# Kernel optimization log

Hardware: AMD Instinct MI355X
Metric: run time of the kernel (lower is better)

Reference implementation:

```python
import jax
import jax.numpy as jnp
from jax import lax
import numpy as np

ALPHA = 1.5   # entmax sparsity parameter (layer default)
N_ITER = 50   # bisection iterations (converges to ~2^-50 interval)


def entmax_bisect(z, alpha=ALPHA, n_iter=N_ITER):
    """alpha-entmax along the last axis via bisection on the threshold tau.

    p_i = max((alpha-1)*z_i - tau, 0) ** (1/(alpha-1)), with sum_i p_i = 1.
    """
    inv = 1.0 / (alpha - 1.0)
    x = (alpha - 1.0) * z
    mx = jnp.max(x, axis=-1, keepdims=True)
    d = x.shape[-1]
    lo = mx - 1.0                      # f(lo) >= 0
    hi = mx - float(d) ** (1.0 - alpha)  # f(hi) <= 0

    def body(_, carry):
        lo, hi = carry
        mid = 0.5 * (lo + hi)
        p = jnp.maximum(x - mid, 0.0) ** inv
        f = jnp.sum(p, axis=-1, keepdims=True) - 1.0
        lo = jnp.where(f >= 0.0, mid, lo)
        hi = jnp.where(f >= 0.0, hi, mid)
        return lo, hi

    lo, hi = lax.fori_loop(0, n_iter, body, (lo, hi))
    tau = 0.5 * (lo + hi)
    p = jnp.maximum(x - tau, 0.0) ** inv
    return p / jnp.sum(p, axis=-1, keepdims=True)


def setup_inputs() -> dict:
    k = jax.random.key(0)
    kq, kk, kv = jax.random.split(k, 3)
    B, S, D = 8, 2048, 128
    return {
        "query": jax.random.normal(kq, (B, S, D), dtype=jnp.float32),
        "key": jax.random.normal(kk, (B, S, D), dtype=jnp.float32),
        "value": jax.random.normal(kv, (B, S, D), dtype=jnp.float32),
    }


def reference(query, key, value):
    # scores: [B, Sq, Sk]
    scores = jnp.einsum("bqd,bkd->bqk", query, key)
    weights = entmax_bisect(scores, alpha=ALPHA)
    # outputs: [B, Sq, D]
    return jnp.einsum("bqk,bkd->bqd", weights, value)
```

## Files before the change

### kernel.cpp

```cpp
#include <hip/hip_runtime.h>
#include <math.h>

#define NB 8
#define S 2048
#define D 128
#define ROWS 32
#define CAP 64
#define NTH 256
#define WKEYS 512
#define CHUNK 32
#define NCK (WKEYS / CHUNK)
#define MARGIN 1.6f

typedef __attribute__((ext_vector_type(8))) short bf16x8;
typedef __attribute__((ext_vector_type(4))) float f32x4;

__device__ __forceinline__ unsigned fmap(float f) {
    unsigned u = __float_as_uint(f);
    return (u & 0x80000000u) ? ~u : (u | 0x80000000u);
}
__device__ __forceinline__ float funmap(unsigned k) {
    return (k & 0x80000000u) ? __uint_as_float(k ^ 0x80000000u) : __uint_as_float(~k);
}
__device__ __forceinline__ unsigned short f2bf(float f) {
    unsigned u = __float_as_uint(f);
    return (unsigned short)((u + 0x7fffu + ((u >> 16) & 1u)) >> 16);
}

__global__ void convert_kernel(const float* __restrict__ q, const float* __restrict__ k,
                               unsigned short* __restrict__ qb, unsigned short* __restrict__ kb) {
    int i = blockIdx.x * NTH + threadIdx.x;
    float4 qv = ((const float4*)q)[i];
    float4 kv = ((const float4*)k)[i];
    ushort4 qo, ko;
    qo.x = f2bf(0.5f * qv.x); qo.y = f2bf(0.5f * qv.y); qo.z = f2bf(0.5f * qv.z); qo.w = f2bf(0.5f * qv.w);
    ko.x = f2bf(kv.x);        ko.y = f2bf(kv.y);        ko.z = f2bf(kv.z);        ko.w = f2bf(kv.w);
    ((ushort4*)qb)[i] = qo;
    ((ushort4*)kb)[i] = ko;
}

__global__ __launch_bounds__(NTH, 2) void entmax_mfma_kernel(
    const float* __restrict__ query, const float* __restrict__ key,
    const float* __restrict__ value, float* __restrict__ out,
    const unsigned short* __restrict__ qb, const unsigned short* __restrict__ kb)
{
    __shared__ float cVal[ROWS][CAP];
    __shared__ unsigned short cIdx[ROWS][CAP];
    __shared__ unsigned rmS[ROWS];
    __shared__ int ccnt[ROWS];

    const int tid  = threadIdx.x;
    const int b    = blockIdx.x & 7;
    const int rb   = blockIdx.x >> 3;
    const int w    = tid >> 6;
    const int lane = tid & 63;
    const int g    = lane >> 4;
    const int l15  = lane & 15;

    if (tid < ROWS) { rmS[tid] = fmap(-3.0e38f); ccnt[tid] = 0; }
    __syncthreads();

    const uint4* Qb4 = (const uint4*)qb + (size_t)(b * S + rb * ROWS) * 16;
    uint4 aq[2][4];
    #pragma unroll
    for (int rt = 0; rt < 2; rt++)
        #pragma unroll
        for (int s = 0; s < 4; s++)
            aq[rt][s] = Qb4[(rt * 16 + l15) * 16 + s * 4 + g];

    const uint4* Kb4 = (const uint4*)kb + (size_t)(b * S) * 16;
    const int key0w = w * WKEYS;

    float rmr[2][4];
    #pragma unroll
    for (int rt = 0; rt < 2; rt++)
        #pragma unroll
        for (int j = 0; j < 4; j++) rmr[rt][j] = -3.0e38f;

    uint4 bb0[8], bb1[8];

#define LOADB(dst, ck_)                                                              \
    {                                                                                \
        int kbase_ = key0w + (ck_) * CHUNK;                                          \
        _Pragma("unroll")                                                            \
        for (int kt = 0; kt < 2; kt++)                                               \
            _Pragma("unroll")                                                        \
            for (int s = 0; s < 4; s++)                                              \
                dst[kt * 4 + s] = Kb4[(size_t)(kbase_ + kt * 16 + l15) * 16 + s * 4 + g]; \
    }

#define CHUNK_BODY(cur, nxt, ck_)                                                    \
    {                                                                                \
        if ((ck_) + 1 < NCK) LOADB(nxt, (ck_) + 1);                                  \
        f32x4 acc[2][2];                                                             \
        _Pragma("unroll")                                                            \
        for (int rt = 0; rt < 2; rt++)                                               \
            _Pragma("unroll")                                                        \
            for (int kt = 0; kt < 2; kt++) acc[rt][kt] = (f32x4){0.f, 0.f, 0.f, 0.f}; \
        _Pragma("unroll")                                                            \
        for (int s = 0; s < 4; s++) {                                                \
            bf16x8 fb0 = *reinterpret_cast<const bf16x8*>(&cur[0 * 4 + s]);          \
            bf16x8 fb1 = *reinterpret_cast<const bf16x8*>(&cur[1 * 4 + s]);          \
            _Pragma("unroll")                                                        \
            for (int rt = 0; rt < 2; rt++) {                                         \
                bf16x8 fa = *reinterpret_cast<const bf16x8*>(&aq[rt][s]);            \
                acc[rt][0] = __builtin_amdgcn_mfma_f32_16x16x32_bf16(fa, fb0, acc[rt][0], 0, 0, 0); \
                acc[rt][1] = __builtin_amdgcn_mfma_f32_16x16x32_bf16(fa, fb1, acc[rt][1], 0, 0, 0); \
            }                                                                        \
        }                                                                            \
          \
        float red[2][4];                                                             \
        _Pragma("unroll")                                                            \
        for (int rt = 0; rt < 2; rt++)                                               \
            _Pragma("unroll")                                                        \
            for (int j = 0; j < 4; j++) red[rt][j] = fmaxf(acc[rt][0][j], acc[rt][1][j]); \
        _Pragma("unroll")                                                            \
        for (int m = 1; m <= 8; m <<= 1)                                             \
            _Pragma("unroll")                                                        \
            for (int rt = 0; rt < 2; rt++)                                           \
                _Pragma("unroll")                                                    \
                for (int j = 0; j < 4; j++)                                          \
                    red[rt][j] = fmaxf(red[rt][j], __shfl_xor(red[rt][j], m));       \
        bool up[2][4];                                                               \
        _Pragma("unroll")                                                            \
        for (int rt = 0; rt < 2; rt++)                                               \
            _Pragma("unroll")                                                        \
            for (int j = 0; j < 4; j++) {                                            \
                up[rt][j] = red[rt][j] > rmr[rt][j];                                 \
                rmr[rt][j] = fmaxf(rmr[rt][j], red[rt][j]);                          \
            }                                                                        \
        if (l15 == 0) {                                                              \
            _Pragma("unroll")                                                        \
            for (int rt = 0; rt < 2; rt++)                                           \
                _Pragma("unroll")                                                    \
                for (int j = 0; j < 4; j++)                                          \
                    if (up[rt][j]) atomicMax(&rmS[rt * 16 + g * 4 + j], fmap(rmr[rt][j])); \
        }                                                                            \
        float thr[2][4];                                                             \
        _Pragma("unroll")                                                            \
        for (int rt = 0; rt < 2; rt++)                                               \
            _Pragma("unroll")                                                        \
            for (int j = 0; j < 4; j++)                                              \
                thr[rt][j] = fmaxf(rmr[rt][j], funmap(rmS[rt * 16 + g * 4 + j])) - MARGIN; \
        int kb0_ = key0w + (ck_) * CHUNK + l15;                                      \
        _Pragma("unroll")                                                            \
        for (int rt = 0; rt < 2; rt++)                                               \
            _Pragma("unroll")                                                        \
            for (int kt = 0; kt < 2; kt++)                                           \
                _Pragma("unroll")                                                    \
                for (int j = 0; j < 4; j++) {                                        \
                    float v_ = acc[rt][kt][j];                                       \
                    if (v_ > thr[rt][j]) {                                           \
                        int row_ = rt * 16 + g * 4 + j;                              \
                        int slot_ = atomicAdd(&ccnt[row_], 1);                       \
                        if (slot_ < CAP) {                                           \
                            cVal[row_][slot_] = v_;                                  \
                            cIdx[row_][slot_] = (unsigned short)(kb0_ + kt * 16);    \
                        }                                                            \
                    }                                                                \
                }                                                                    \
    }

    LOADB(bb0, 0);
    for (int t = 0; t < NCK / 2; t++) {
        CHUNK_BODY(bb0, bb1, 2 * t);
        CHUNK_BODY(bb1, bb0, 2 * t + 1);
    }

    if (l15 == 0) {
        #pragma unroll
        for (int rt = 0; rt < 2; rt++)
            #pragma unroll
            for (int j = 0; j < 4; j++)
                atomicMax(&rmS[rt * 16 + g * 4 + j], fmap(rmr[rt][j]));
    }
    __syncthreads();

    const float* Qg = query + (size_t)(b * S + rb * ROWS) * D;
    const float* Kg = key   + (size_t)b * S * D;
    const float* Vg = value + (size_t)b * S * D;
    float* Og = out + (size_t)(b * S + rb * ROWS) * D;

    for (int r8 = 0; r8 < 8; r8++) {
        int row = w * 8 + r8;
        int n = min(ccnt[row], CAP);
        float thrc = funmap(rmS[row]) - MARGIN;

        float v = (lane < n) ? cVal[row][lane] : -3.0e38f;
        unsigned short id = (lane < n) ? cIdx[row][lane] : 0;
        unsigned long long mk = __ballot(v > thrc);
        int nc = __popcll(mk);
        int pos = __popcll(mk & ((1ull << lane) - 1ull));
        if (v > thrc) cIdx[row][pos] = id;

        int c0 = lane >> 3;
        int dl = lane & 7;
        float4 q4[4];
        #pragma unroll
        for (int i = 0; i < 4; i++)
            q4[i] = ((const float4*)(Qg + (size_t)row * D))[dl * 4 + i];
        for (int cc = c0; cc < nc; cc += 8) {
            int ky = cIdx[row][cc];
            float s = 0.f;
            #pragma unroll
            for (int i = 0; i < 4; i++) {
                float4 k4 = ((const float4*)(Kg + (size_t)ky * D))[dl * 4 + i];
                s = fmaf(q4[i].x, k4.x, s);
                s = fmaf(q4[i].y, k4.y, s);
                s = fmaf(q4[i].z, k4.z, s);
                s = fmaf(q4[i].w, k4.w, s);
            }
            s += __shfl_xor(s, 1);
            s += __shfl_xor(s, 2);
            s += __shfl_xor(s, 4);
            if (dl == 0) cVal[row][cc] = 0.5f * s;
        }

        float tauf = 0.f;
        if (lane == 0) {
            for (int i = 0; i < nc - 1; i++) {
                int mi = i; float mv = cVal[row][i];
                for (int j2 = i + 1; j2 < nc; j2++)
                    if (cVal[row][j2] > mv) { mv = cVal[row][j2]; mi = j2; }
                if (mi != i) {
                    float tv = cVal[row][i]; cVal[row][i] = cVal[row][mi]; cVal[row][mi] = tv;
                    unsigned short ti = cIdx[row][i]; cIdx[row][i] = cIdx[row][mi]; cIdx[row][mi] = ti;
                }
            }
            double S1 = 0.0, S2 = 0.0;
            double tau = (double)cVal[row][0] - 1.0;
            for (int k2 = 1; k2 <= nc; k2++) {
                double xk = (double)cVal[row][k2 - 1];
                S1 += xk; S2 += xk * xk;
                double disc = S1 * S1 - (double)k2 * (S2 - 1.0);
                if (disc >= 0.0) {
                    double tk = (S1 - sqrt(disc)) / (double)k2;
                    if (xk > tk) tau = tk;
                }
            }
            tauf = (float)tau;
        }
        tauf = __shfl(tauf, 0);

        float Z = 0.f;
        float2 o = make_float2(0.f, 0.f);
        for (int cc = 0; cc < nc; cc++) {
            float x = cVal[row][cc];
            float t = fmaxf(x - tauf, 0.f);
            float p = t * t;
            Z += p;
            if (t > 0.f) {
                int ky = cIdx[row][cc];
                float2 a = ((const float2*)(Vg + (size_t)ky * D))[lane];
                o.x = fmaf(p, a.x, o.x);
                o.y = fmaf(p, a.y, o.y);
            }
        }
        float zi = 1.0f / Z;
        o.x *= zi; o.y *= zi;
        ((float2*)(Og + (size_t)row * D))[lane] = o;
    }
}

#define FTK 64
#define FNT (S / FTK)
#define FCAP 120
#define HI_OFF 0.022097086912079608f
#define NITER 50

__global__ __launch_bounds__(NTH, 2) void entmax_attn_fallback(
    const float* __restrict__ query, const float* __restrict__ key,
    const float* __restrict__ value, float* __restrict__ out)
{
    __shared__ float4 sK[FTK * 32];
    __shared__ float4 sQ[ROWS * 32];
    __shared__ int    cIdx[ROWS][FCAP];
    __shared__ float  cVal[ROWS][FCAP];
    __shared__ int    ccnt[ROWS];

    const int tid = threadIdx.x;
    const int bid = blockIdx.x;
    const int b   = bid >> 6;
    const int rb  = bid & 63;

    const float4* Qg = (const float4*)(query + ((size_t)b * S + (size_t)rb * ROWS) * D);
    const float4* Kg = (const float4*)(key + (size_t)b * S * D);

    #pragma unroll
    for (int i = 0; i < 4; i++) {
        int f = tid + NTH * i;
        float4 v = Qg[f];
        v.x *= 0.5f; v.y *= 0.5f; v.z *= 0.5f; v.w *= 0.5f;
        sQ[f] = v;
    }
    if (tid < ROWS) ccnt[tid] = 0;

    const int kg  = tid & 31;
    const int rg  = tid >> 5;
    const int swz = kg & 7;

    float rm[4];
    #pragma unroll
    for (int i = 0; i < 4; i++) rm[i] = -3.0e38f;

    float4 pre[8];
    #pragma unroll
    for (int i = 0; i < 8; i++) pre[i] = Kg[tid + NTH * i];

    for (int t = 0; t < FNT; t++) {
        #pragma unroll
        for (int i = 0; i < 8; i++) {
            int f = tid + NTH * i;
            int kl = f >> 5, dc = f & 31;
            sK[kl * 32 + (dc ^ (kl & 7))] = pre[i];
        }
        if (t + 1 < FNT) {
            #pragma unroll
            for (int i = 0; i < 8; i++) pre[i] = Kg[(t + 1) * (FTK * 32) + tid + NTH * i];
        }
        __syncthreads();

        float acc[4][2] = {{0.f,0.f},{0.f,0.f},{0.f,0.f},{0.f,0.f}};
        #pragma unroll 8
        for (int dc = 0; dc < 32; dc++) {
            int sw = dc ^ swz;
            float4 k0 = sK[kg * 32 + sw];
            float4 k1 = sK[(kg + 32) * 32 + sw];
            #pragma unroll
            for (int i = 0; i < 4; i++) {
                float4 qv = sQ[(rg * 4 + i) * 32 + dc];
                acc[i][0] = fmaf(qv.x, k0.x, acc[i][0]);
                acc[i][0] = fmaf(qv.y, k0.y, acc[i][0]);
                acc[i][0] = fmaf(qv.z, k0.z, acc[i][0]);
                acc[i][0] = fmaf(qv.w, k0.w, acc[i][0]);
                acc[i][1] = fmaf(qv.x, k1.x, acc[i][1]);
                acc[i][1] = fmaf(qv.y, k1.y, acc[i][1]);
                acc[i][1] = fmaf(qv.z, k1.z, acc[i][1]);
                acc[i][1] = fmaf(qv.w, k1.w, acc[i][1]);
            }
        }

        #pragma unroll
        for (int i = 0; i < 4; i++) {
            float m = fmaxf(acc[i][0], acc[i][1]);
            m = fmaxf(m, __shfl_xor(m, 1));
            m = fmaxf(m, __shfl_xor(m, 2));
            m = fmaxf(m, __shfl_xor(m, 4));
            m = fmaxf(m, __shfl_xor(m, 8));
            m = fmaxf(m, __shfl_xor(m, 16));
            rm[i] = fmaxf(rm[i], m);
            float thr = rm[i] - 1.0f;
            #pragma unroll
            for (int j = 0; j < 2; j++) {
                if (acc[i][j] > thr) {
                    int row = rg * 4 + i;
                    int slot = atomicAdd(&ccnt[row], 1);
                    if (slot < FCAP) {
                        cIdx[row][slot] = t * FTK + kg + 32 * j;
                        cVal[row][slot] = acc[i][j];
                    }
                }
            }
        }
        __syncthreads();
    }

    const int wid  = tid >> 6;
    const int lane = tid & 63;
    const float* Vb = value + (size_t)b * S * D;
    float* Ob = out + ((size_t)b * S + (size_t)rb * ROWS) * D;

    #pragma unroll
    for (int r8 = 0; r8 < 8; r8++) {
        int row = wid * 8 + r8;
        int n = min(ccnt[row], FCAP);
        float mx = __shfl(rm[r8 & 3], (r8 & 4) ? 32 : 0);

        float lo = mx - 1.0f;
        float hi = mx - HI_OFF;
        for (int it = 0; it < NITER; it++) {
            float mid = 0.5f * (lo + hi);
            float s = 0.0f;
            for (int c = lane; c < n; c += 64) {
                float tv = fmaxf(cVal[row][c] - mid, 0.0f);
                s = fmaf(tv, tv, s);
            }
            s += __shfl_xor(s, 1); s += __shfl_xor(s, 2); s += __shfl_xor(s, 4);
            s += __shfl_xor(s, 8); s += __shfl_xor(s, 16); s += __shfl_xor(s, 32);
            if (s - 1.0f >= 0.0f) lo = mid; else hi = mid;
        }
        float tau = 0.5f * (lo + hi);

        float z = 0.0f;
        for (int c = lane; c < n; c += 64) {
            float tv = fmaxf(cVal[row][c] - tau, 0.0f);
            float p = tv * tv;
            cVal[row][c] = p;
            z += p;
        }
        z += __shfl_xor(z, 1); z += __shfl_xor(z, 2); z += __shfl_xor(z, 4);
        z += __shfl_xor(z, 8); z += __shfl_xor(z, 16); z += __shfl_xor(z, 32);
        float zinv = 1.0f / z;

        float2 o = make_float2(0.0f, 0.0f);
        for (int c = 0; c < n; c++) {
            float p = cVal[row][c];
            int ii = cIdx[row][c];
            float2 a = ((const float2*)(Vb + (size_t)ii * D))[lane];
            o.x = fmaf(p, a.x, o.x); o.y = fmaf(p, a.y, o.y);
        }
        o.x *= zinv; o.y *= zinv;
        ((float2*)(Ob + (size_t)row * D))[lane] = o;
    }
}

extern "C" void kernel_launch(void* const* d_in, const int* in_sizes, int n_in,
                              void* d_out, int out_size, void* d_ws, size_t ws_size,
                              hipStream_t stream) {
    const float* q = (const float*)d_in[0];
    const float* k = (const float*)d_in[1];
    const float* v = (const float*)d_in[2];
    float* o = (float*)d_out;

    const size_t nelem = (size_t)NB * S * D;
    const size_t ws_needed = 2 * nelem * sizeof(unsigned short);

    if (ws_size >= ws_needed) {
        unsigned short* qb = (unsigned short*)d_ws;
        unsigned short* kb = qb + nelem;
        hipLaunchKernelGGL(convert_kernel, dim3(nelem / 4 / NTH), dim3(NTH), 0, stream,
                           q, k, qb, kb);
        hipLaunchKernelGGL(entmax_mfma_kernel, dim3(NB * (S / ROWS)), dim3(NTH), 0, stream,
                           q, k, v, o, qb, kb);
    } else {
        hipLaunchKernelGGL(entmax_attn_fallback, dim3(NB * (S / ROWS)), dim3(NTH), 0, stream,
                           q, k, v, o);
    }
}
```

Measured before the change: 147.9 us.

## Fuse bf16 conversion of Q/K into the MFMA entmax kernel

Removes the separate convert kernel and workspace path; the main kernel now loads fp32 query/key directly and packs them to bf16 in registers before the MFMA calls. This eliminates one launch and the write/read round trip of bf16 copies. The cost is that each block now reads K as fp32 (twice the bytes) and does the conversion redundantly across the 512 blocks per batch, with larger prefetch register arrays that may pressure occupancy. The fallback kernel is dropped.

```diff
diff --git a/kernel.cpp b/kernel.cpp
--- a/kernel.cpp
+++ b/kernel.cpp
@@ -26,23 +26,22 @@
     unsigned u = __float_as_uint(f);
     return (unsigned short)((u + 0x7fffu + ((u >> 16) & 1u)) >> 16);
 }
-
-__global__ void convert_kernel(const float* __restrict__ q, const float* __restrict__ k,
-                               unsigned short* __restrict__ qb, unsigned short* __restrict__ kb) {
-    int i = blockIdx.x * NTH + threadIdx.x;
-    float4 qv = ((const float4*)q)[i];
-    float4 kv = ((const float4*)k)[i];
-    ushort4 qo, ko;
-    qo.x = f2bf(0.5f * qv.x); qo.y = f2bf(0.5f * qv.y); qo.z = f2bf(0.5f * qv.z); qo.w = f2bf(0.5f * qv.w);
-    ko.x = f2bf(kv.x);        ko.y = f2bf(kv.y);        ko.z = f2bf(kv.z);        ko.w = f2bf(kv.w);
-    ((ushort4*)qb)[i] = qo;
-    ((ushort4*)kb)[i] = ko;
-}
-
-__global__ __launch_bounds__(NTH, 2) void entmax_mfma_kernel(
+__device__ __forceinline__ bf16x8 pack8(const float4 a, const float4 b, const float sc) {
+    bf16x8 r;
+    r[0] = (short)f2bf(sc * a.x);
+    r[1] = (short)f2bf(sc * a.y);
+    r[2] = (short)f2bf(sc * a.z);
+    r[3] = (short)f2bf(sc * a.w);
+    r[4] = (short)f2bf(sc * b.x);
+    r[5] = (short)f2bf(sc * b.y);
+    r[6] = (short)f2bf(sc * b.z);
+    r[7] = (short)f2bf(sc * b.w);
+    return r;
+}
+
+__global__ __launch_bounds__(NTH, 2) void entmax_fused2_kernel(
     const float* __restrict__ query, const float* __restrict__ key,
-    const float* __restrict__ value, float* __restrict__ out,
-    const unsigned short* __restrict__ qb, const unsigned short* __restrict__ kb)
+    const float* __restrict__ value, float* __restrict__ out)
 {
     __shared__ float cVal[ROWS][CAP];
     __shared__ unsigned short cIdx[ROWS][CAP];
@@ -60,15 +59,18 @@
     if (tid < ROWS) { rmS[tid] = fmap(-3.0e38f); ccnt[tid] = 0; }
     __syncthreads();
 
-    const uint4* Qb4 = (const uint4*)qb + (size_t)(b * S + rb * ROWS) * 16;
-    uint4 aq[2][4];
+    const float4* QF4 = (const float4*)(query + (size_t)(b * S + rb * ROWS) * D);
+    const float4* KF4 = (const float4*)(key + (size_t)b * S * D);
+
+    bf16x8 aq[2][4];
     #pragma unroll
     for (int rt = 0; rt < 2; rt++)
         #pragma unroll
-        for (int s = 0; s < 4; s++)
-            aq[rt][s] = Qb4[(rt * 16 + l15) * 16 + s * 4 + g];
-
-    const uint4* Kb4 = (const uint4*)kb + (size_t)(b * S) * 16;
+        for (int s = 0; s < 4; s++) {
+            const float4* P = QF4 + (rt * 16 + l15) * 32 + s * 8 + g * 2;
+            aq[rt][s] = pack8(P[0], P[1], 0.5f);
+        }
+
     const int key0w = w * WKEYS;
 
     float rmr[2][4];
@@ -77,20 +79,30 @@
         #pragma unroll
         for (int j = 0; j < 4; j++) rmr[rt][j] = -3.0e38f;
 
-    uint4 bb0[8], bb1[8];
+    float4 raw0[16], raw1[16];
 
 #define LOADB(dst, ck_)                                                              \
     {                                                                                \
-        int kbase_ = key0w + (ck_) * CHUNK;                                          \
         _Pragma("unroll")                                                            \
         for (int kt = 0; kt < 2; kt++)                                               \
             _Pragma("unroll")                                                        \
-            for (int s = 0; s < 4; s++)                                              \
-                dst[kt * 4 + s] = Kb4[(size_t)(kbase_ + kt * 16 + l15) * 16 + s * 4 + g]; \
+            for (int s = 0; s < 4; s++) {                                            \
+                const float4* P_ = KF4 +                                             \
+                    (size_t)(key0w + (ck_) * CHUNK + kt * 16 + l15) * 32 + s * 8 + g * 2; \
+                dst[kt * 8 + s * 2 + 0] = P_[0];                                     \
+                dst[kt * 8 + s * 2 + 1] = P_[1];                                     \
+            }                                                                        \
     }
 
 #define CHUNK_BODY(cur, nxt, ck_)                                                    \
     {                                                                                \
+               \
+        bf16x8 fb[2][4];                                                             \
+        _Pragma("unroll")                                                            \
+        for (int kt = 0; kt < 2; kt++)                                               \
+            _Pragma("unroll")                                                        \
+            for (int s = 0; s < 4; s++)                                              \
+                fb[kt][s] = pack8(cur[kt * 8 + s * 2], cur[kt * 8 + s * 2 + 1], 1.0f); \
         if ((ck_) + 1 < NCK) LOADB(nxt, (ck_) + 1);                                  \
         f32x4 acc[2][2];                                                             \
         _Pragma("unroll")                                                            \
@@ -99,16 +111,13 @@
             for (int kt = 0; kt < 2; kt++) acc[rt][kt] = (f32x4){0.f, 0.f, 0.f, 0.f}; \
         _Pragma("unroll")                                                            \
         for (int s = 0; s < 4; s++) {                                                \
-            bf16x8 fb0 = *reinterpret_cast<const bf16x8*>(&cur[0 * 4 + s]);          \
-            bf16x8 fb1 = *reinterpret_cast<const bf16x8*>(&cur[1 * 4 + s]);          \
             _Pragma("unroll")                                                        \
             for (int rt = 0; rt < 2; rt++) {                                         \
-                bf16x8 fa = *reinterpret_cast<const bf16x8*>(&aq[rt][s]);            \
-                acc[rt][0] = __builtin_amdgcn_mfma_f32_16x16x32_bf16(fa, fb0, acc[rt][0], 0, 0, 0); \
-                acc[rt][1] = __builtin_amdgcn_mfma_f32_16x16x32_bf16(fa, fb1, acc[rt][1], 0, 0, 0); \
+                acc[rt][0] = __builtin_amdgcn_mfma_f32_16x16x32_bf16(aq[rt][s], fb[0][s], acc[rt][0], 0, 0, 0); \
+                acc[rt][1] = __builtin_amdgcn_mfma_f32_16x16x32_bf16(aq[rt][s], fb[1][s], acc[rt][1], 0, 0, 0); \
             }                                                                        \
         }                                                                            \
-          \
+         \
         float red[2][4];                                                             \
         _Pragma("unroll")                                                            \
         for (int rt = 0; rt < 2; rt++)                                               \
@@ -161,10 +170,10 @@
                 }                                                                    \
     }
 
-    LOADB(bb0, 0);
+    LOADB(raw0, 0);
     for (int t = 0; t < NCK / 2; t++) {
-        CHUNK_BODY(bb0, bb1, 2 * t);
-        CHUNK_BODY(bb1, bb0, 2 * t + 1);
+        CHUNK_BODY(raw0, raw1, 2 * t);
+        CHUNK_BODY(raw1, raw0, 2 * t + 1);
     }
 
     if (l15 == 0) {
@@ -257,160 +266,7 @@
             }
         }
         float zi = 1.0f / Z;
-        o.x *= zi; o.y *= zi;
-        ((float2*)(Og + (size_t)row * D))[lane] = o;
-    }
-}
-
-#define FTK 64
-#define FNT (S / FTK)
-#define FCAP 120
-#define HI_OFF 0.022097086912079608f
-#define NITER 50
-
-__global__ __launch_bounds__(NTH, 2) void entmax_attn_fallback(
-    const float* __restrict__ query, const float* __restrict__ key,
-    const float* __restrict__ value, float* __restrict__ out)
-{
-    __shared__ float4 sK[FTK * 32];
-    __shared__ float4 sQ[ROWS * 32];
-    __shared__ int    cIdx[ROWS][FCAP];
-    __shared__ float  cVal[ROWS][FCAP];
-    __shared__ int    ccnt[ROWS];
-
-    const int tid = threadIdx.x;
-    const int bid = blockIdx.x;
-    const int b   = bid >> 6;
-    const int rb  = bid & 63;
-
-    const float4* Qg = (const float4*)(query + ((size_t)b * S + (size_t)rb * ROWS) * D);
-    const float4* Kg = (const float4*)(key + (size_t)b * S * D);
-
-    #pragma unroll
-    for (int i = 0; i < 4; i++) {
-        int f = tid + NTH * i;
-        float4 v = Qg[f];
-        v.x *= 0.5f; v.y *= 0.5f; v.z *= 0.5f; v.w *= 0.5f;
-        sQ[f] = v;
-    }
-    if (tid < ROWS) ccnt[tid] = 0;
-
-    const int kg  = tid & 31;
-    const int rg  = tid >> 5;
-    const int swz = kg & 7;
-
-    float rm[4];
-    #pragma unroll
-    for (int i = 0; i < 4; i++) rm[i] = -3.0e38f;
-
-    float4 pre[8];
-    #pragma unroll
-    for (int i = 0; i < 8; i++) pre[i] = Kg[tid + NTH * i];
-
-    for (int t = 0; t < FNT; t++) {
-        #pragma unroll
-        for (int i = 0; i < 8; i++) {
-            int f = tid + NTH * i;
-            int kl = f >> 5, dc = f & 31;
-            sK[kl * 32 + (dc ^ (kl & 7))] = pre[i];
-        }
-        if (t + 1 < FNT) {
-            #pragma unroll
-            for (int i = 0; i < 8; i++) pre[i] = Kg[(t + 1) * (FTK * 32) + tid + NTH * i];
-        }
-        __syncthreads();
-
-        float acc[4][2] = {{0.f,0.f},{0.f,0.f},{0.f,0.f},{0.f,0.f}};
-        #pragma unroll 8
-        for (int dc = 0; dc < 32; dc++) {
-            int sw = dc ^ swz;
-            float4 k0 = sK[kg * 32 + sw];
-            float4 k1 = sK[(kg + 32) * 32 + sw];
-            #pragma unroll
-            for (int i = 0; i < 4; i++) {
-                float4 qv = sQ[(rg * 4 + i) * 32 + dc];
-                acc[i][0] = fmaf(qv.x, k0.x, acc[i][0]);
-                acc[i][0] = fmaf(qv.y, k0.y, acc[i][0]);
-                acc[i][0] = fmaf(qv.z, k0.z, acc[i][0]);
-                acc[i][0] = fmaf(qv.w, k0.w, acc[i][0]);
-                acc[i][1] = fmaf(qv.x, k1.x, acc[i][1]);
-                acc[i][1] = fmaf(qv.y, k1.y, acc[i][1]);
-                acc[i][1] = fmaf(qv.z, k1.z, acc[i][1]);
-                acc[i][1] = fmaf(qv.w, k1.w, acc[i][1]);
-            }
-        }
-
-        #pragma unroll
-        for (int i = 0; i < 4; i++) {
-            float m = fmaxf(acc[i][0], acc[i][1]);
-            m = fmaxf(m, __shfl_xor(m, 1));
-            m = fmaxf(m, __shfl_xor(m, 2));
-            m = fmaxf(m, __shfl_xor(m, 4));
-            m = fmaxf(m, __shfl_xor(m, 8));
-            m = fmaxf(m, __shfl_xor(m, 16));
-            rm[i] = fmaxf(rm[i], m);
-            float thr = rm[i] - 1.0f;
-            #pragma unroll
-            for (int j = 0; j < 2; j++) {
-                if (acc[i][j] > thr) {
-                    int row = rg * 4 + i;
-                    int slot = atomicAdd(&ccnt[row], 1);
-                    if (slot < FCAP) {
-                        cIdx[row][slot] = t * FTK + kg + 32 * j;
-                        cVal[row][slot] = acc[i][j];
-                    }
-                }
-            }
-        }
-        __syncthreads();
-    }
-
-    const int wid  = tid >> 6;
-    const int lane = tid & 63;
-    const float* Vb = value + (size_t)b * S * D;
-    float* Ob = out + ((size_t)b * S + (size_t)rb * ROWS) * D;
-
-    #pragma unroll
-    for (int r8 = 0; r8 < 8; r8++) {
-        int row = wid * 8 + r8;
-        int n = min(ccnt[row], FCAP);
-        float mx = __shfl(rm[r8 & 3], (r8 & 4) ? 32 : 0);
-
-        float lo = mx - 1.0f;
-        float hi = mx - HI_OFF;
-        for (int it = 0; it < NITER; it++) {
-            float mid = 0.5f * (lo + hi);
-            float s = 0.0f;
-            for (int c = lane; c < n; c += 64) {
-                float tv = fmaxf(cVal[row][c] - mid, 0.0f);
-                s = fmaf(tv, tv, s);
-            }
-            s += __shfl_xor(s, 1); s += __shfl_xor(s, 2); s += __shfl_xor(s, 4);
-            s += __shfl_xor(s, 8); s += __shfl_xor(s, 16); s += __shfl_xor(s, 32);
-            if (s - 1.0f >= 0.0f) lo = mid; else hi = mid;
-        }
-        float tau = 0.5f * (lo + hi);
-
-        float z = 0.0f;
-        for (int c = lane; c < n; c += 64) {
-            float tv = fmaxf(cVal[row][c] - tau, 0.0f);
-            float p = tv * tv;
-            cVal[row][c] = p;
-            z += p;
-        }
-        z += __shfl_xor(z, 1); z += __shfl_xor(z, 2); z += __shfl_xor(z, 4);
-        z += __shfl_xor(z, 8); z += __shfl_xor(z, 16); z += __shfl_xor(z, 32);
-        float zinv = 1.0f / z;
-
-        float2 o = make_float2(0.0f, 0.0f);
-        for (int c = 0; c < n; c++) {
-            float p = cVal[row][c];
-            int ii = cIdx[row][c];
-            float2 a = ((const float2*)(Vb + (size_t)ii * D))[lane];
-            o.x = fmaf(p, a.x, o.x); o.y = fmaf(p, a.y, o.y);
-        }
-        o.x *= zinv; o.y *= zinv;
-        ((float2*)(Ob + (size_t)row * D))[lane] = o;
+        ((float2*)(Og + (size_t)row * D))[lane] = make_float2(o.x * zi, o.y * zi);
     }
 }
 
@@ -421,19 +277,7 @@
     const float* k = (const float*)d_in[1];
     const float* v = (const float*)d_in[2];
     float* o = (float*)d_out;
-
-    const size_t nelem = (size_t)NB * S * D;
-    const size_t ws_needed = 2 * nelem * sizeof(unsigned short);
-
-    if (ws_size >= ws_needed) {
-        unsigned short* qb = (unsigned short*)d_ws;
-        unsigned short* kb = qb + nelem;
-        hipLaunchKernelGGL(convert_kernel, dim3(nelem / 4 / NTH), dim3(NTH), 0, stream,
-                           q, k, qb, kb);
-        hipLaunchKernelGGL(entmax_mfma_kernel, dim3(NB * (S / ROWS)), dim3(NTH), 0, stream,
-                           q, k, v, o, qb, kb);
-    } else {
-        hipLaunchKernelGGL(entmax_attn_fallback, dim3(NB * (S / ROWS)), dim3(NTH), 0, stream,
-                           q, k, v, o);
-    }
-}
+    dim3 grid(NB * (S / ROWS));
+    dim3 block(NTH);
+    hipLaunchKernelGGL(entmax_fused2_kernel, grid, block, 0, stream, q, k, v, o);
+}
```

Measured after the change: 170.0 us. 15.0% more time.
